# Optimization experiments

Measured on AMD Instinct MI355X. Metric: run time of the kernel, lower is better.

Reference implementation:

```python
import jax, jax.numpy as jnp
import numpy as np

L, DIM, H, DH, MUL = 4, 1024, 16, 64, 4
INNER = H * DH
HID = DIM * MUL
EPS = 1e-5


def setup_inputs() -> dict:
    key = jax.random.key(0)
    ks = jax.random.split(key, 16)
    s = 0.02
    inp = {
        "x": jax.random.normal(ks[0], (2, 2048, DIM), dtype=jnp.float32),
        "ln1_g": jnp.ones((L, DIM), jnp.float32),
        "ln1_b": jnp.zeros((L, DIM), jnp.float32),
        "Wq": jax.random.normal(ks[1], (L, DIM, INNER), jnp.float32) * s,
        "Wk": jax.random.normal(ks[2], (L, DIM, INNER), jnp.float32) * s,
        "Wv": jax.random.normal(ks[3], (L, DIM, INNER), jnp.float32) * s,
        "Wo": jax.random.normal(ks[4], (L, INNER, DIM), jnp.float32) * s,
        "ln3_g": jnp.ones((L, DIM), jnp.float32),
        "ln3_b": jnp.zeros((L, DIM), jnp.float32),
        "fc1_w": jax.random.normal(ks[5], (L, DIM, HID), jnp.float32) * s,
        "fc1_b": jnp.zeros((L, HID), jnp.float32),
        "fc2_w": jax.random.normal(ks[6], (L, HID, DIM), jnp.float32) * s,
        "fc2_b": jnp.zeros((L, DIM), jnp.float32),
    }
    return inp


def _layernorm(x, g, b):
    mu = jnp.mean(x, axis=-1, keepdims=True)
    var = jnp.var(x, axis=-1, keepdims=True)
    return (x - mu) * jax.lax.rsqrt(var + EPS) * g + b


def _attention(xn, wq, wk, wv, wo):
    B, S, _ = xn.shape
    q = (xn @ wq).reshape(B, S, H, DH).transpose(0, 2, 1, 3)  # b h s d
    k = (xn @ wk).reshape(B, S, H, DH).transpose(0, 2, 1, 3)
    v = (xn @ wv).reshape(B, S, H, DH).transpose(0, 2, 1, 3)
    scale = DH ** -0.5
    sim = jnp.einsum("bhid,bhjd->bhij", q, k) * scale
    mask = jnp.triu(jnp.ones((S, S), dtype=bool), k=1)
    sim = jnp.where(mask, jnp.finfo(sim.dtype).min, sim)
    attn = jax.nn.softmax(sim, axis=-1)
    out = jnp.einsum("bhij,bhjd->bhid", attn, v)
    out = out.transpose(0, 2, 1, 3).reshape(B, S, INNER)
    return out @ wo


def reference(x, ln1_g, ln1_b, Wq, Wk, Wv, Wo, ln3_g, ln3_b, fc1_w, fc1_b, fc2_w, fc2_b):
    for l in range(L):
        x = x + _attention(_layernorm(x, ln1_g[l], ln1_b[l]), Wq[l], Wk[l], Wv[l], Wo[l])
        h = _layernorm(x, ln3_g[l], ln3_b[l])
        h = jax.nn.gelu(h @ fc1_w[l] + fc1_b[l], approximate=False)
        x = x + (h @ fc2_w[l] + fc2_b[l])
    return x
```

## Files before the change

### kernel.cpp

```cpp
#include <hip/hip_runtime.h>

typedef unsigned short u16;
typedef unsigned int u32;
typedef __attribute__((ext_vector_type(8))) short short8;
typedef __attribute__((ext_vector_type(4))) float f32x4;
typedef __attribute__((ext_vector_type(4))) unsigned short u16x4;

__device__ inline u16 f2bf(float f) {
  u32 u = __builtin_bit_cast(u32, f);
  u32 r = (u + 0x7fffu + ((u >> 16) & 1u)) >> 16;
  return (u16)r;
}

__device__ inline void gload16(const void* g, void* l) {
  __builtin_amdgcn_global_load_lds((const __attribute__((address_space(1))) void*)g,
                                   (__attribute__((address_space(3))) void*)l, 16, 0, 0);
}

__global__ __launch_bounds__(256) void transpose_cast(
    const float* __restrict__ src, u16* __restrict__ dst, int K, int N)
{
  __shared__ u16 tile[64][72];
  int bk = blockIdx.x * 64, bn = blockIdx.y * 64;
  int t = threadIdx.x;
  int r = t >> 2, c0 = (t & 3) * 16;
  const float* sp = src + (size_t)(bk + r) * N + bn + c0;
#pragma unroll
  for (int j = 0; j < 16; j += 4) {
    float4 v = *(const float4*)(sp + j);
    tile[r][c0 + j + 0] = f2bf(v.x);
    tile[r][c0 + j + 1] = f2bf(v.y);
    tile[r][c0 + j + 2] = f2bf(v.z);
    tile[r][c0 + j + 3] = f2bf(v.w);
  }
  __syncthreads();
  int nr = t >> 2, k0 = (t & 3) * 16;
  u16* dp = dst + (size_t)(bn + nr) * K + bk + k0;
  short8 v0, v1;
#pragma unroll
  for (int j = 0; j < 8; ++j) v0[j] = (short)tile[k0 + j][nr];
#pragma unroll
  for (int j = 0; j < 8; ++j) v1[j] = (short)tile[k0 + 8 + j][nr];
  *(short8*)dp = v0;
  *(short8*)(dp + 8) = v1;
}

__global__ __launch_bounds__(256) void vtranspose(
    const u16* __restrict__ qkv, u16* __restrict__ vtb)
{
  __shared__ u16 tile[64][72];
  int bt = blockIdx.x;
  int bh = blockIdx.y;
  int b = bh >> 4, h = bh & 15;
  const u16* src = qkv + (size_t)b * 2048 * 3072 + 2048 + h * 64;
  u16* dst = vtb + (size_t)bh * 64 * 2048;
  int t = threadIdx.x;
  int r = t >> 2, c0 = (t & 3) * 16;
  const u16* sp = src + (size_t)(bt * 64 + r) * 3072 + c0;
  *(short8*)&tile[r][c0] = *(const short8*)sp;
  *(short8*)&tile[r][c0 + 8] = *(const short8*)(sp + 8);
  __syncthreads();
  int nr = t >> 2, k0 = (t & 3) * 16;
  u16* dp = dst + (size_t)nr * 2048 + bt * 64 + k0;
  short8 v0, v1;
#pragma unroll
  for (int j = 0; j < 8; ++j) v0[j] = (short)tile[k0 + j][nr];
#pragma unroll
  for (int j = 0; j < 8; ++j) v1[j] = (short)tile[k0 + 8 + j][nr];
  *(short8*)dp = v0;
  *(short8*)(dp + 8) = v1;
}

__global__ __launch_bounds__(256) void ln_kernel(
    const float* __restrict__ x, const float* __restrict__ g,
    const float* __restrict__ be, u16* __restrict__ out)
{
  int row = blockIdx.x;
  int t = threadIdx.x;
  const float4* xr = (const float4*)(x + (size_t)row * 1024);
  float4 v = xr[t];
  float s = v.x + v.y + v.z + v.w;
  float ss = v.x * v.x + v.y * v.y + v.z * v.z + v.w * v.w;
#pragma unroll
  for (int off = 1; off < 64; off <<= 1) {
    s += __shfl_xor(s, off);
    ss += __shfl_xor(ss, off);
  }
  __shared__ float red[8];
  int w = t >> 6, lane = t & 63;
  if (lane == 0) { red[w * 2] = s; red[w * 2 + 1] = ss; }
  __syncthreads();
  s = red[0] + red[2] + red[4] + red[6];
  ss = red[1] + red[3] + red[5] + red[7];
  float mu = s * (1.0f / 1024.0f);
  float var = ss * (1.0f / 1024.0f) - mu * mu;
  float rs = rsqrtf(var + 1e-5f);
  float4 gg = ((const float4*)g)[t];
  float4 bb = ((const float4*)be)[t];
  u16x4 o;
  o[0] = f2bf((v.x - mu) * rs * gg.x + bb.x);
  o[1] = f2bf((v.y - mu) * rs * gg.y + bb.y);
  o[2] = f2bf((v.z - mu) * rs * gg.z + bb.z);
  o[3] = f2bf((v.w - mu) * rs * gg.w + bb.w);
  ((u16x4*)(out + (size_t)row * 1024))[t] = o;
}

template <int EPI, int BN>
__global__ __launch_bounds__(256) void gemm_bf16(
    const u16* __restrict__ A, const u16* __restrict__ Bt,
    u16* __restrict__ C, const float* __restrict__ bias, float* X,
    int M, int N, int K)
{
  constexpr int NJ = BN / 32;
  __shared__ __align__(16) u16 As[128 * 32];
  __shared__ __align__(16) u16 Bs[BN * 32];
  int bm = blockIdx.x * 128, bn = blockIdx.y * BN;
  int tid = threadIdx.x;
  int w = tid >> 6, lane = tid & 63;
  int wm = (w >> 1) * 64, wn = (w & 1) * (BN / 2);
  int frow = lane & 15, fk = (lane >> 4) * 8;

  f32x4 acc[4][NJ];
#pragma unroll
  for (int i = 0; i < 4; ++i)
#pragma unroll
    for (int j = 0; j < NJ; ++j) acc[i][j] = (f32x4){0.f, 0.f, 0.f, 0.f};

  int ca0 = tid, ca1 = tid + 256;
  int ar0 = ca0 >> 2, ak0 = (ca0 & 3) * 8;
  int ar1 = ca1 >> 2, ak1 = (ca1 & 3) * 8;
  const u16* Abase = A + (size_t)bm * K;
  const u16* Bbase = Bt + (size_t)bn * K;
  u16* As0 = As + (size_t)(w * 64) * 8;
  u16* As1 = As + (size_t)(256 + w * 64) * 8;
  u16* Bs0 = Bs + (size_t)(w * 64) * 8;
  u16* Bs1 = Bs + (size_t)(256 + w * 64) * 8;

  for (int k0 = 0; k0 < K; k0 += 32) {
    __syncthreads();
    gload16(Abase + (size_t)ar0 * K + k0 + ak0, As0);
    gload16(Abase + (size_t)ar1 * K + k0 + ak1, As1);
    gload16(Bbase + (size_t)ar0 * K + k0 + ak0, Bs0);
    if constexpr (BN == 128) gload16(Bbase + (size_t)ar1 * K + k0 + ak1, Bs1);
    __syncthreads();

    short8 a[4], b[NJ];
#pragma unroll
    for (int i = 0; i < 4; ++i) a[i] = *(const short8*)&As[(wm + i * 16 + frow) * 32 + fk];
#pragma unroll
    for (int j = 0; j < NJ; ++j) b[j] = *(const short8*)&Bs[(wn + j * 16 + frow) * 32 + fk];
#pragma unroll
    for (int i = 0; i < 4; ++i)
#pragma unroll
      for (int j = 0; j < NJ; ++j)
        acc[i][j] = __builtin_amdgcn_mfma_f32_16x16x32_bf16(a[i], b[j], acc[i][j], 0, 0, 0);
  }

  int r0 = (lane >> 4) * 4;
#pragma unroll
  for (int i = 0; i < 4; ++i) {
#pragma unroll
    for (int r = 0; r < 4; ++r) {
      int gr = bm + wm + i * 16 + r0 + r;
      size_t rowb = (size_t)gr * N;
#pragma unroll
      for (int j = 0; j < NJ; ++j) {
        int gc = bn + wn + j * 16 + frow;
        float v = acc[i][j][r];
        if constexpr (EPI == 0) {
          C[rowb + gc] = f2bf(v);
        } else if constexpr (EPI == 1) {
          v += bias[gc];
          v = 0.5f * v * (1.0f + erff(v * 0.70710678118654752f));
          C[rowb + gc] = f2bf(v);
        } else {
          if (bias) v += bias[gc];
          X[rowb + gc] += v;
        }
      }
    }
  }
}

__global__ __launch_bounds__(256) void flash_attn3(
    const u16* __restrict__ qkv, const u16* __restrict__ vtb, u16* __restrict__ ao)
{
  const int SEQ = 2048, LDQ = 3072;
  const float SCL2 = 0.18033688011112042f;
  int ib = blockIdx.x;
  int qb = (ib < 256) ? (15 - (ib >> 5)) : ((ib - 256) >> 5);
  int bh = ib & 31;
  int b = bh >> 4, h = bh & 15;
  size_t base = (size_t)b * SEQ * LDQ;
  const u16* Qp = qkv + base + h * 64;
  const u16* Kp = qkv + base + 1024 + h * 64;
  const u16* Vtp = vtb + (size_t)bh * 64 * SEQ;

  __shared__ __align__(16) u16 Kt[64][72];
  __shared__ __align__(16) u16 Vt[64][72];
  __shared__ __align__(16) u16 Pl[4][32][72];

  int tid = threadIdx.x;
  int w = tid >> 6, lane = tid & 63;
  int frow = lane & 15, fkh = lane >> 4;
  int fk = fkh * 8;
  int qbase = qb * 128 + w * 32;

  short8 qf[2][2];
#pragma unroll
  for (int qi = 0; qi < 2; ++qi) {
    const u16* qr = Qp + (size_t)(qbase + qi * 16 + frow) * LDQ;
    qf[qi][0] = *(const short8*)(qr + fk);
    qf[qi][1] = *(const short8*)(qr + 32 + fk);
  }

  short8 ones;
#pragma unroll
  for (int j = 0; j < 8; ++j) ones[j] = (short)0x3F80;

  f32x4 o[2][4];
  f32x4 lacc[2];
  float mrow[2][4];
#pragma unroll
  for (int qi = 0; qi < 2; ++qi) {
    lacc[qi] = (f32x4){0.f, 0.f, 0.f, 0.f};
#pragma unroll
    for (int nf = 0; nf < 4; ++nf) o[qi][nf] = (f32x4){0.f, 0.f, 0.f, 0.f};
#pragma unroll
    for (int r = 0; r < 4; ++r) mrow[qi][r] = -1e30f;
  }

  int sr0 = tid >> 3, sc0 = (tid & 7) * 8;
  int sr1 = (tid + 256) >> 3, sc1 = ((tid + 256) & 7) * 8;

  int ntiles = qb * 2 + 2;
  for (int jb = 0; jb < ntiles; ++jb) {
    __syncthreads();
    *(short8*)&Kt[sr0][sc0] = *(const short8*)(Kp + (size_t)(jb * 64 + sr0) * LDQ + sc0);
    *(short8*)&Kt[sr1][sc1] = *(const short8*)(Kp + (size_t)(jb * 64 + sr1) * LDQ + sc1);
    *(short8*)&Vt[sr0][sc0] = *(const short8*)(Vtp + (size_t)sr0 * SEQ + jb * 64 + sc0);
    *(short8*)&Vt[sr1][sc1] = *(const short8*)(Vtp + (size_t)sr1 * SEQ + jb * 64 + sc1);
    __syncthreads();

    short8 kf[4][2];
#pragma unroll
    for (int nf = 0; nf < 4; ++nf) {
      kf[nf][0] = *(const short8*)&Kt[nf * 16 + frow][fk];
      kf[nf][1] = *(const short8*)&Kt[nf * 16 + frow][32 + fk];
    }

#pragma unroll
    for (int qi = 0; qi < 2; ++qi) {
      f32x4 s[4];
#pragma unroll
      for (int nf = 0; nf < 4; ++nf) s[nf] = (f32x4){0.f, 0.f, 0.f, 0.f};
#pragma unroll
      for (int nf = 0; nf < 4; ++nf) {
        s[nf] = __builtin_amdgcn_mfma_f32_16x16x32_bf16(qf[qi][0], kf[nf][0], s[nf], 0, 0, 0);
        s[nf] = __builtin_amdgcn_mfma_f32_16x16x32_bf16(qf[qi][1], kf[nf][1], s[nf], 0, 0, 0);
      }

      float pv[4][4];
#pragma unroll
      for (int nf = 0; nf < 4; ++nf)
#pragma unroll
        for (int r = 0; r < 4; ++r) pv[nf][r] = s[nf][r] * SCL2;

      bool needmask = (jb * 64 + 63) > (qbase + qi * 16);
      if (needmask) {
#pragma unroll
        for (int nf = 0; nf < 4; ++nf)
#pragma unroll
          for (int r = 0; r < 4; ++r) {
            int tok = jb * 64 + nf * 16 + frow;
            int qr = qbase + qi * 16 + fkh * 4 + r;
            if (tok > qr) pv[nf][r] = -1e30f;
          }
      }

      float rmax[4] = {-1e30f, -1e30f, -1e30f, -1e30f};
#pragma unroll
      for (int nf = 0; nf < 4; ++nf)
#pragma unroll
        for (int r = 0; r < 4; ++r) rmax[r] = fmaxf(rmax[r], pv[nf][r]);
#pragma unroll
      for (int off = 1; off < 16; off <<= 1) {
#pragma unroll
        for (int r = 0; r < 4; ++r) rmax[r] = fmaxf(rmax[r], __shfl_xor(rmax[r], off));
      }

      float g = -1e30f;
#pragma unroll
      for (int r = 0; r < 4; ++r) g = fmaxf(g, rmax[r] - mrow[qi][r]);
      if (__any(g > 12.0f)) {
#pragma unroll
        for (int r = 0; r < 4; ++r) {
          float mn = fmaxf(mrow[qi][r], rmax[r]);
          float sc = exp2f(mrow[qi][r] - mn);
          mrow[qi][r] = mn;
          lacc[qi][r] *= sc;
#pragma unroll
          for (int nf = 0; nf < 4; ++nf) o[qi][nf][r] *= sc;
        }
      }

#pragma unroll
      for (int nf = 0; nf < 4; ++nf)
#pragma unroll
        for (int r = 0; r < 4; ++r) {
          float p = exp2f(pv[nf][r] - mrow[qi][r]);
          Pl[w][qi * 16 + fkh * 4 + r][nf * 16 + frow] = f2bf(p);
        }
    }

    asm volatile("s_waitcnt lgkmcnt(0)" ::: "memory");
#pragma unroll
    for (int ks = 0; ks < 2; ++ks) {
      short8 pa0 = *(const short8*)&Pl[w][frow][ks * 32 + fk];
      short8 pa1 = *(const short8*)&Pl[w][16 + frow][ks * 32 + fk];
      lacc[0] = __builtin_amdgcn_mfma_f32_16x16x32_bf16(pa0, ones, lacc[0], 0, 0, 0);
      lacc[1] = __builtin_amdgcn_mfma_f32_16x16x32_bf16(pa1, ones, lacc[1], 0, 0, 0);
#pragma unroll
      for (int nf = 0; nf < 4; ++nf) {
        short8 vb = *(const short8*)&Vt[nf * 16 + frow][ks * 32 + fk];
        o[0][nf] = __builtin_amdgcn_mfma_f32_16x16x32_bf16(pa0, vb, o[0][nf], 0, 0, 0);
        o[1][nf] = __builtin_amdgcn_mfma_f32_16x16x32_bf16(pa1, vb, o[1][nf], 0, 0, 0);
      }
    }
  }

#pragma unroll
  for (int qi = 0; qi < 2; ++qi) {
#pragma unroll
    for (int nf = 0; nf < 4; ++nf) {
#pragma unroll
      for (int r = 0; r < 4; ++r) {
        int qr = qbase + qi * 16 + fkh * 4 + r;
        int dc = nf * 16 + frow;
        ao[((size_t)b * SEQ + qr) * 1024 + h * 64 + dc] = f2bf(o[qi][nf][r] / lacc[qi][r]);
      }
    }
  }
}

extern "C" void kernel_launch(void* const* d_in, const int* in_sizes, int n_in,
                              void* d_out, int out_size, void* d_ws, size_t ws_size,
                              hipStream_t stream)
{
  const float* x_in = (const float*)d_in[0];
  const float* ln1g = (const float*)d_in[1];
  const float* ln1b = (const float*)d_in[2];
  const float* Wq   = (const float*)d_in[3];
  const float* Wk   = (const float*)d_in[4];
  const float* Wv   = (const float*)d_in[5];
  const float* Wo   = (const float*)d_in[6];
  const float* ln3g = (const float*)d_in[7];
  const float* ln3b = (const float*)d_in[8];
  const float* fc1w = (const float*)d_in[9];
  const float* fc1b = (const float*)d_in[10];
  const float* fc2w = (const float*)d_in[11];
  const float* fc2b = (const float*)d_in[12];

  float* xbuf = (float*)d_out;

  char* ws = (char*)d_ws;
  size_t off = 0;
  u16* xn     = (u16*)(ws + off);  off += (size_t)4096 * 1024 * 2;
  u16* qkvb   = (u16*)(ws + off);  off += (size_t)4096 * 3072 * 2;
  u16* aob    = (u16*)(ws + off);  off += (size_t)4096 * 1024 * 2;
  u16* hbuf   = qkvb;
  u16* vtb    = (u16*)(ws + off);  off += (size_t)32 * 64 * 2048 * 2;
  u16* wqkv_l = (u16*)(ws + off);  off += (size_t)3072 * 1024 * 2;
  u16* wo_l   = (u16*)(ws + off);  off += (size_t)1024 * 1024 * 2;
  u16* wfc1_l = (u16*)(ws + off);  off += (size_t)4096 * 1024 * 2;
  u16* wfc2_l = (u16*)(ws + off);  off += (size_t)1024 * 4096 * 2;

  hipMemcpyAsync(xbuf, x_in, (size_t)4096 * 1024 * 4, hipMemcpyDeviceToDevice, stream);

  dim3 blk(256);
  for (int l = 0; l < 4; ++l) {
    transpose_cast<<<dim3(16, 16), blk, 0, stream>>>(Wq + (size_t)l * 1024 * 1024, wqkv_l,                        1024, 1024);
    transpose_cast<<<dim3(16, 16), blk, 0, stream>>>(Wk + (size_t)l * 1024 * 1024, wqkv_l + (size_t)1024 * 1024,  1024, 1024);
    transpose_cast<<<dim3(16, 16), blk, 0, stream>>>(Wv + (size_t)l * 1024 * 1024, wqkv_l + (size_t)2048 * 1024,  1024, 1024);
    transpose_cast<<<dim3(16, 16), blk, 0, stream>>>(Wo + (size_t)l * 1024 * 1024, wo_l,                          1024, 1024);
    transpose_cast<<<dim3(16, 64), blk, 0, stream>>>(fc1w + (size_t)l * 1024 * 4096, wfc1_l,                      1024, 4096);
    transpose_cast<<<dim3(64, 16), blk, 0, stream>>>(fc2w + (size_t)l * 4096 * 1024, wfc2_l,                      4096, 1024);

    ln_kernel<<<4096, blk, 0, stream>>>(xbuf, ln1g + l * 1024, ln1b + l * 1024, xn);
    gemm_bf16<0, 128><<<dim3(32, 24), blk, 0, stream>>>(xn, wqkv_l, qkvb, nullptr, nullptr, 4096, 3072, 1024);
    vtranspose<<<dim3(32, 32), blk, 0, stream>>>(qkvb, vtb);
    flash_attn3<<<dim3(512), blk, 0, stream>>>(qkvb, vtb, aob);
    gemm_bf16<2, 64><<<dim3(32, 16), blk, 0, stream>>>(aob, wo_l, nullptr, nullptr, xbuf, 4096, 1024, 1024);
    ln_kernel<<<4096, blk, 0, stream>>>(xbuf, ln3g + l * 1024, ln3b + l * 1024, xn);
    gemm_bf16<1, 128><<<dim3(32, 32), blk, 0, stream>>>(xn, wfc1_l, hbuf, fc1b + l * 4096, nullptr, 4096, 4096, 1024);
    gemm_bf16<2, 64><<<dim3(32, 16), blk, 0, stream>>>(hbuf, wfc2_l, nullptr, fc2b + l * 1024, xbuf, 4096, 1024, 4096);
  }
}
```

Baseline: 1.382 ms.

## Double-buffer GEMM LDS tiles and XOR-swizzle K chunks to avoid bank conflicts

The bf16 GEMM now keeps two LDS buffers for A and B. It issues the async global-to-LDS loads for the next K tile before computing on the current one, so each iteration needs one barrier instead of two. The global source K-chunk is also XOR-swizzled by row, with matching read offsets precomputed per lane, to reduce LDS bank conflicts on the short8 fragment reads. LDS use doubles, which may lower occupancy. Correctness relies on the barrier also waiting for the outstanding LDS-bound loads.

```diff
diff --git a/kernel.cpp b/kernel.cpp
--- a/kernel.cpp
+++ b/kernel.cpp
@@ -112,13 +112,13 @@
     int M, int N, int K)
 {
   constexpr int NJ = BN / 32;
-  __shared__ __align__(16) u16 As[128 * 32];
-  __shared__ __align__(16) u16 Bs[BN * 32];
+  __shared__ __align__(16) u16 As[2][128 * 32];
+  __shared__ __align__(16) u16 Bs[2][BN * 32];
   int bm = blockIdx.x * 128, bn = blockIdx.y * BN;
   int tid = threadIdx.x;
   int w = tid >> 6, lane = tid & 63;
   int wm = (w >> 1) * 64, wn = (w & 1) * (BN / 2);
-  int frow = lane & 15, fk = (lane >> 4) * 8;
+  int frow = lane & 15, fkb = lane >> 4;
 
   f32x4 acc[4][NJ];
 #pragma unroll
@@ -127,34 +127,53 @@
     for (int j = 0; j < NJ; ++j) acc[i][j] = (f32x4){0.f, 0.f, 0.f, 0.f};
 
   int ca0 = tid, ca1 = tid + 256;
-  int ar0 = ca0 >> 2, ak0 = (ca0 & 3) * 8;
-  int ar1 = ca1 >> 2, ak1 = (ca1 & 3) * 8;
+  int ar0 = ca0 >> 2, ak0 = (((ca0 & 3) ^ ((ar0 >> 1) & 3))) * 8;
+  int ar1 = ca1 >> 2, ak1 = (((ca1 & 3) ^ ((ar1 >> 1) & 3))) * 8;
   const u16* Abase = A + (size_t)bm * K;
   const u16* Bbase = Bt + (size_t)bn * K;
-  u16* As0 = As + (size_t)(w * 64) * 8;
-  u16* As1 = As + (size_t)(256 + w * 64) * 8;
-  u16* Bs0 = Bs + (size_t)(w * 64) * 8;
-  u16* Bs1 = Bs + (size_t)(256 + w * 64) * 8;
-
-  for (int k0 = 0; k0 < K; k0 += 32) {
-    __syncthreads();
-    gload16(Abase + (size_t)ar0 * K + k0 + ak0, As0);
-    gload16(Abase + (size_t)ar1 * K + k0 + ak1, As1);
-    gload16(Bbase + (size_t)ar0 * K + k0 + ak0, Bs0);
-    if constexpr (BN == 128) gload16(Bbase + (size_t)ar1 * K + k0 + ak1, Bs1);
-    __syncthreads();
-
+
+  int offa[4], offb[NJ];
+#pragma unroll
+  for (int i = 0; i < 4; ++i) {
+    int row = wm + i * 16 + frow;
+    offa[i] = row * 32 + ((fkb ^ ((row >> 1) & 3)) * 8);
+  }
+#pragma unroll
+  for (int j = 0; j < NJ; ++j) {
+    int row = wn + j * 16 + frow;
+    offb[j] = row * 32 + ((fkb ^ ((row >> 1) & 3)) * 8);
+  }
+
+  int nt = K >> 5;
+
+#define STAGE(buf, k0)                                                              \
+  do {                                                                              \
+    gload16(Abase + (size_t)ar0 * K + (k0) + ak0, &As[buf][(size_t)(w * 64) * 8]);  \
+    gload16(Abase + (size_t)ar1 * K + (k0) + ak1, &As[buf][(size_t)(256 + w * 64) * 8]); \
+    gload16(Bbase + (size_t)ar0 * K + (k0) + ak0, &Bs[buf][(size_t)(w * 64) * 8]);  \
+    if constexpr (BN == 128)                                                        \
+      gload16(Bbase + (size_t)ar1 * K + (k0) + ak1, &Bs[buf][(size_t)(256 + w * 64) * 8]); \
+  } while (0)
+
+  STAGE(0, 0);
+  __syncthreads();
+  int cur = 0;
+  for (int t = 0; t < nt; ++t) {
+    if (t + 1 < nt) STAGE(cur ^ 1, (t + 1) * 32);
     short8 a[4], b[NJ];
 #pragma unroll
-    for (int i = 0; i < 4; ++i) a[i] = *(const short8*)&As[(wm + i * 16 + frow) * 32 + fk];
-#pragma unroll
-    for (int j = 0; j < NJ; ++j) b[j] = *(const short8*)&Bs[(wn + j * 16 + frow) * 32 + fk];
+    for (int i = 0; i < 4; ++i) a[i] = *(const short8*)&As[cur][offa[i]];
+#pragma unroll
+    for (int j = 0; j < NJ; ++j) b[j] = *(const short8*)&Bs[cur][offb[j]];
 #pragma unroll
     for (int i = 0; i < 4; ++i)
 #pragma unroll
       for (int j = 0; j < NJ; ++j)
         acc[i][j] = __builtin_amdgcn_mfma_f32_16x16x32_bf16(a[i], b[j], acc[i][j], 0, 0, 0);
-  }
+    __syncthreads();
+    cur ^= 1;
+  }
+#undef STAGE
 
   int r0 = (lane >> 4) * 4;
 #pragma unroll
```

After: 1.293 ms. -6.4%, faster.
